# Performance work log

Measured on AMD Instinct MI355X. Metric: run time of the kernel, lower is better.

Reference implementation:

```python
import jax, jax.numpy as jnp
import numpy as np

N = 50000      # nodes
E = 800000     # edges
IN_DIM = 256
HID = 96
OUT = 64
K = 2
ALPHA = 0.15
SCALING = 1.8  # NormalizedGCNConv scaling_factor
EPS = 1e-12    # torch F.normalize eps


def setup_inputs() -> dict:
    key = jax.random.key(0)
    ks = jax.random.split(key, 8)
    x = jax.random.normal(ks[0], (N, IN_DIM), jnp.float32)
    edge_index = jax.random.randint(ks[1], (2, E), 0, N, dtype=jnp.int64)
    def lin(k, fi, fo):
        s = 1.0 / np.sqrt(fi)
        kw, kb = jax.random.split(k)
        W = jax.random.uniform(kw, (fi, fo), jnp.float32, -s, s)
        b = jax.random.uniform(kb, (fo,), jnp.float32, -s, s)
        return W, b
    W0, b0 = lin(ks[2], IN_DIM, HID)   # convs[0]
    W1, b1 = lin(ks[3], HID, HID)      # convs[1]
    Wx, bx = lin(ks[4], HID, OUT)      # convx
    return {"x": x, "edge_index": edge_index,
            "W0": W0, "b0": b0, "W1": W1, "b1": b1, "Wx": Wx, "bx": bx}


def _l2norm(x):
    n = jnp.linalg.norm(x, axis=1, keepdims=True)
    return x / jnp.maximum(n, EPS)


def _gcn_norm(edge_index):
    # add self loops, symmetric normalization D^-1/2 (A+I) D^-1/2
    loop = jnp.arange(N, dtype=edge_index.dtype)
    row = jnp.concatenate([edge_index[0], loop])
    col = jnp.concatenate([edge_index[1], loop])
    deg = jax.ops.segment_sum(jnp.ones(row.shape[0], jnp.float32), col, num_segments=N)
    dinv = jnp.where(deg > 0, jax.lax.rsqrt(jnp.maximum(deg, 1.0)), 0.0)
    norm = dinv[row] * dinv[col]   # [E+N]
    return row, col, norm


def _norm_gcn_conv(x, W, b, row, col, norm):
    # linear -> L2 normalize * 1.8 -> APPNP(K, alpha), eval mode (no dropout)
    x = x @ W + b
    x = _l2norm(x) * SCALING
    h = x
    for _ in range(K):
        agg = jax.ops.segment_sum(x[row] * norm[:, None], col, num_segments=N)
        x = (1.0 - ALPHA) * agg + ALPHA * h
    return x


def reference(x, edge_index, W0, b0, W1, b1, Wx, bx):
    row, col, norm = _gcn_norm(edge_index)
    out = jax.nn.relu(_norm_gcn_conv(x, W0, b0, row, col, norm))
    # depth=3, link_len=2: loop runs i=1 only, residual condition never fires
    out = _l2norm(_norm_gcn_conv(out, W1, b1, row, col, norm)) * 1.5
    return _norm_gcn_conv(out, Wx, bx, row, col, norm)
```

## Files before the change

### kernel.cpp

```cpp
#include <hip/hip_runtime.h>
#include <hip/hip_fp16.h>
#include <math.h>

#define BETA_C 0.85f
#define ALF_C  0.15f
#define SLOTS 48

typedef _Float16 f16x8 __attribute__((ext_vector_type(8)));
typedef float f32x4 __attribute__((ext_vector_type(4)));

__device__ inline f16x8 as_h8(uint4 v) { union { uint4 u; f16x8 h; } U; U.u = v; return U.h; }

__global__ __launch_bounds__(256) void k_fill_tlp(
        const int* __restrict__ row, const int* __restrict__ col,
        int* __restrict__ cur, int* __restrict__ adj, int E, unsigned mulc) {
    int cls = blockIdx.x & 7;
    int e = (blockIdx.x >> 3) * 256 + threadIdx.x;
    if (e >= E) return;
    int c = col[e];
    if ((int)(((unsigned long long)(unsigned)c * mulc) >> 32) != cls) return;
    int p = atomicAdd(&cur[c], 1);
    if (p < SLOTS) adj[(size_t)c * SLOTS + p] = row[e];
}

__global__ void k_prep(const int* __restrict__ cur, float2* __restrict__ dinv2,
                       int* __restrict__ adj, int n, int t0,
                       const float* __restrict__ W0, const float* __restrict__ W1,
                       const float* __restrict__ Wx, ushort* __restrict__ WT0,
                       ushort* __restrict__ WT1, ushort* __restrict__ WTx) {
    int idx = blockIdx.x * blockDim.x + threadIdx.x;
    if (idx < n) {
        int deg = cur[idx];
        float degf = (float)deg + 1.0f;
        dinv2[idx] = make_float2(rsqrtf(degf), ALF_C * sqrtf(degf));
        int ds = min(deg, SLOTS);
        int d4 = (ds + 3) & ~3;
        int* ap = adj + (size_t)idx * SLOTS;
        for (int p = ds; p < d4; ++p) ap[p] = idx;
    } else if (idx >= t0) {
        const int S0 = 96 * 256, S1 = 96 * 96, S2 = 64 * 96;
        int li = idx - t0;
        const float* W; ushort* WT; int FI, FO;
        if (li < S0)           { W = W0; WT = WT0; FI = 256; FO = 96; }
        else if (li < S0 + S1) { W = W1; WT = WT1; FI = 96;  FO = 96; li -= S0; }
        else if (li < S0+S1+S2){ W = Wx; WT = WTx; FI = 96;  FO = 64; li -= S0 + S1; }
        else return;
        int nrow = li / FI, k = li % FI;
        _Float16 hv = (_Float16)W[(size_t)k * FO + nrow];
        WT[li] = *(ushort*)&hv;
    }
}

template<int FI, int FO, int ASRC_F16>
__global__ __launch_bounds__(256) void k_gemm_mfma(
        const void* __restrict__ Xv, const ushort* __restrict__ WT,
        const float* __restrict__ Bias, const float2* __restrict__ dinv2,
        ushort* __restrict__ H, int n, float scale) {
    constexpr int NT = FO / 16;
    constexpr int CPR = FI / 8;
    __shared__ ushort sA[64 * FI];
    __shared__ ushort sW[FO * FI];
    const int tid = threadIdx.x;
    const int rb = blockIdx.x * 64;

    {
        constexpr int TOT = FO * CPR;
#pragma unroll
        for (int idx = tid; idx < TOT; idx += 256) {
            int nrow = idx / CPR, c = idx % CPR;
            uint4 v = *(((const uint4*)WT) + (size_t)nrow * CPR + c);
            int byte = ((nrow * FI + c * 8) * 2) ^ ((nrow & 7) << 4);
            *(uint4*)((char*)sW + byte) = v;
        }
    }
    {
        constexpr int TOT = 64 * CPR;
#pragma unroll
        for (int idx = tid; idx < TOT; idx += 256) {
            int r = idx / CPR, c = idx % CPR;
            int gr = rb + r;
            uint4 v = make_uint4(0u, 0u, 0u, 0u);
            if (ASRC_F16) {
                if (gr < n) v = *(((const uint4*)Xv) + (size_t)gr * CPR + c);
            } else {
                if (gr < n) {
                    const float4* Xp = (const float4*)Xv;
                    float4 f0 = Xp[(size_t)gr * (FI / 4) + c * 2];
                    float4 f1 = Xp[(size_t)gr * (FI / 4) + c * 2 + 1];
                    _Float16 hv[8] = {(_Float16)f0.x, (_Float16)f0.y, (_Float16)f0.z,
                                      (_Float16)f0.w, (_Float16)f1.x, (_Float16)f1.y,
                                      (_Float16)f1.z, (_Float16)f1.w};
                    v = *(uint4*)hv;
                }
            }
            int byte = ((r * FI + c * 8) * 2) ^ ((r & 7) << 4);
            *(uint4*)((char*)sA + byte) = v;
        }
    }
    __syncthreads();

    const int lane = tid & 63;
    const int wave = tid >> 6;
    const int lcol = lane & 15;
    const int lk = lane >> 4;

    f32x4 acc[NT];
#pragma unroll
    for (int t = 0; t < NT; ++t) acc[t] = (f32x4){0.f, 0.f, 0.f, 0.f};

    const int arow = wave * 16 + lcol;
    char* sAb = (char*)sA;
    char* sWb = (char*)sW;
#pragma unroll
    for (int s = 0; s < FI / 32; ++s) {
        int abyte = ((arow * FI + s * 32 + lk * 8) * 2) ^ ((arow & 7) << 4);
        f16x8 af = *(f16x8*)(sAb + abyte);
#pragma unroll
        for (int t = 0; t < NT; ++t) {
            int nrow = t * 16 + lcol;
            int bbyte = ((nrow * FI + s * 32 + lk * 8) * 2) ^ ((nrow & 7) << 4);
            f16x8 bf = *(f16x8*)(sWb + bbyte);
            acc[t] = __builtin_amdgcn_mfma_f32_16x16x32_f16(af, bf, acc[t], 0, 0, 0);
        }
    }

    float bv[NT];
#pragma unroll
    for (int t = 0; t < NT; ++t) bv[t] = Bias[t * 16 + lcol];
    float ss[4] = {0.f, 0.f, 0.f, 0.f};
#pragma unroll
    for (int t = 0; t < NT; ++t)
#pragma unroll
        for (int r = 0; r < 4; ++r) {
            acc[t][r] += bv[t];
            ss[r] += acc[t][r] * acc[t][r];
        }
    for (int m = 1; m < 16; m <<= 1) {
#pragma unroll
        for (int r = 0; r < 4; ++r) ss[r] += __shfl_xor(ss[r], m, 64);
    }
#pragma unroll
    for (int r = 0; r < 4; ++r) {
        int grow = rb + wave * 16 + lk * 4 + r;
        if (grow < n) {
            float sc = scale * dinv2[grow].x / fmaxf(sqrtf(ss[r]), 1e-12f);
#pragma unroll
            for (int t = 0; t < NT; ++t) {
                _Float16 hv = (_Float16)(acc[t][r] * sc);
                H[(size_t)grow * FO + t * 16 + lcol] = *(ushort*)&hv;
            }
        }
    }
}

__device__ inline void unpack8(uint4 v, float* f) {
    union { uint4 u; _Float16 h[8]; } U; U.u = v;
#pragma unroll
    for (int i = 0; i < 8; ++i) f[i] = (float)U.h[i];
}

template<int C8>
__device__ inline void gather_h(const uint4* __restrict__ tab,
                                const int* __restrict__ ap,
                                int d4, int j, f16x8& A0, f16x8& A1) {
    const int4* ap4 = (const int4*)ap;
    int e = 0;
    for (; e + 8 <= d4; e += 8) {
        int4 a0 = ap4[e >> 2];
        int4 a1 = ap4[(e >> 2) + 1];
        uint4 v0 = tab[(size_t)(unsigned)a0.x * C8 + j];
        uint4 v1 = tab[(size_t)(unsigned)a0.y * C8 + j];
        uint4 v2 = tab[(size_t)(unsigned)a0.z * C8 + j];
        uint4 v3 = tab[(size_t)(unsigned)a0.w * C8 + j];
        uint4 v4 = tab[(size_t)(unsigned)a1.x * C8 + j];
        uint4 v5 = tab[(size_t)(unsigned)a1.y * C8 + j];
        uint4 v6 = tab[(size_t)(unsigned)a1.z * C8 + j];
        uint4 v7 = tab[(size_t)(unsigned)a1.w * C8 + j];
        A0 += (as_h8(v0) + as_h8(v1)) + (as_h8(v2) + as_h8(v3));
        A1 += (as_h8(v4) + as_h8(v5)) + (as_h8(v6) + as_h8(v7));
    }
    if (e < d4) {
        int4 a0 = ap4[e >> 2];
        uint4 v0 = tab[(size_t)(unsigned)a0.x * C8 + j];
        uint4 v1 = tab[(size_t)(unsigned)a0.y * C8 + j];
        uint4 v2 = tab[(size_t)(unsigned)a0.z * C8 + j];
        uint4 v3 = tab[(size_t)(unsigned)a0.w * C8 + j];
        A0 += as_h8(v0) + as_h8(v1);
        A1 += as_h8(v2) + as_h8(v3);
    }
}

template<int C8, int TPB>
__global__ __launch_bounds__(TPB) void k_prop1(
        const uint4* __restrict__ y0, uint4* __restrict__ y1,
        const int* __restrict__ adj, const int* __restrict__ cnt,
        const float2* __restrict__ dinv2, int n) {
    int tid = threadIdx.x;
    int j = tid % C8, cl = tid / C8;
    int c = blockIdx.x * (TPB / C8) + cl;
    if (c >= n) return;
    uint4 sv = y0[(size_t)c * C8 + j];
    float d = dinv2[c].x;
    float a = BETA_C * d * d;
    int deg = min(cnt[c], SLOTS);
    int d4 = (deg + 3) & ~3;
    float coef_s = (a + ALF_C) - a * (float)(d4 - deg);
    f16x8 A0 = {0, 0, 0, 0, 0, 0, 0, 0};
    f16x8 A1 = {0, 0, 0, 0, 0, 0, 0, 0};
    gather_h<C8>(y0, adj + (size_t)c * SLOTS, d4, j, A0, A1);
    float sf[8];
    unpack8(sv, sf);
    _Float16 hv[8];
#pragma unroll
    for (int i = 0; i < 8; ++i) {
        float acc = (float)A0[i] + (float)A1[i];
        hv[i] = (_Float16)(a * acc + coef_s * sf[i]);
    }
    y1[(size_t)c * C8 + j] = *(uint4*)hv;
}

template<int C8, int TPB, int ACT, int OUTF32, int NORM>
__global__ __launch_bounds__(TPB) void k_prop2(
        const uint4* __restrict__ y1, const uint4* __restrict__ y0,
        void* __restrict__ out, const int* __restrict__ adj,
        const int* __restrict__ cnt, const float2* __restrict__ dinv2,
        int n, float nscale) {
    __shared__ float ssh[NORM ? TPB : 1];
    int tid = threadIdx.x;
    int j = tid % C8, cl = tid / C8;
    int c = blockIdx.x * (TPB / C8) + cl;
    if (!NORM && c >= n) return;
    bool on = !NORM || c < n;
    float res[8] = {0, 0, 0, 0, 0, 0, 0, 0};
    if (on) {
        uint4 sv1 = y1[(size_t)c * C8 + j];
        uint4 sv0 = y0[(size_t)c * C8 + j];
        float2 dv = dinv2[c];
        float a = BETA_C * dv.x;
        float t = dv.y;
        int deg = min(cnt[c], SLOTS);
        int d4 = (deg + 3) & ~3;
        float coef_s = a * (1.0f - (float)(d4 - deg));
        f16x8 A0 = {0, 0, 0, 0, 0, 0, 0, 0};
        f16x8 A1 = {0, 0, 0, 0, 0, 0, 0, 0};
        gather_h<C8>(y1, adj + (size_t)c * SLOTS, d4, j, A0, A1);
        float sf[8], tf[8];
        unpack8(sv1, sf);
        unpack8(sv0, tf);
#pragma unroll
        for (int i = 0; i < 8; ++i) {
            float acc = (float)A0[i] + (float)A1[i];
            res[i] = a * acc + coef_s * sf[i] + t * tf[i];
            if (ACT) res[i] = fmaxf(res[i], 0.f);
        }
    }
    if (NORM) {
        float part = 0.f;
#pragma unroll
        for (int i = 0; i < 8; ++i) part += res[i] * res[i];
        ssh[tid] = part;
        __syncthreads();
        if (!on) return;
        float tot = 0.f;
#pragma unroll
        for (int q = 0; q < C8; ++q) tot += ssh[cl * C8 + q];
        float sc = nscale / fmaxf(sqrtf(tot), 1e-12f);
        _Float16 hv[8];
#pragma unroll
        for (int i = 0; i < 8; ++i) hv[i] = (_Float16)(res[i] * sc);
        ((uint4*)out)[(size_t)c * C8 + j] = *(uint4*)hv;
    } else if (OUTF32) {
        float4* op = (float4*)out;
        op[(size_t)c * (C8 * 2) + j * 2]     = make_float4(res[0], res[1], res[2], res[3]);
        op[(size_t)c * (C8 * 2) + j * 2 + 1] = make_float4(res[4], res[5], res[6], res[7]);
    } else {
        _Float16 hv[8];
#pragma unroll
        for (int i = 0; i < 8; ++i) hv[i] = (_Float16)res[i];
        ((uint4*)out)[(size_t)c * C8 + j] = *(uint4*)hv;
    }
}

extern "C" void kernel_launch(void* const* d_in, const int* in_sizes, int n_in,
                              void* d_out, int out_size, void* d_ws, size_t ws_size,
                              hipStream_t stream) {
    const float* x  = (const float*)d_in[0];
    const int*   ei = (const int*)d_in[1];
    const float* W0 = (const float*)d_in[2];
    const float* b0 = (const float*)d_in[3];
    const float* W1 = (const float*)d_in[4];
    const float* b1 = (const float*)d_in[5];
    const float* Wx = (const float*)d_in[6];
    const float* bx = (const float*)d_in[7];
    float* out = (float*)d_out;

    const int N = in_sizes[0] / 256;
    const int E = in_sizes[1] / 2;
    const int* row = ei;
    const int* col = ei + E;

    char* ws = (char*)d_ws;
    size_t off = 0;
    auto alloc = [&](size_t bytes) -> char* {
        char* p = ws + off;
        off += (bytes + 255) & ~(size_t)255;
        return p;
    };
    int*    cur   = (int*)alloc((size_t)N * 4);
    float2* dinv2 = (float2*)alloc((size_t)N * 8);
    int*    adj   = (int*)alloc((size_t)N * SLOTS * 4);
    ushort* WT0   = (ushort*)alloc((size_t)96 * 256 * 2);
    ushort* WT1   = (ushort*)alloc((size_t)96 * 96 * 2);
    ushort* WTx   = (ushort*)alloc((size_t)64 * 96 * 2);
    ushort* Hh    = (ushort*)alloc((size_t)N * 96 * 2);
    ushort* T1h   = (ushort*)alloc((size_t)N * 96 * 2);
    ushort* T2h   = (ushort*)alloc((size_t)N * 96 * 2);
    (void)ws_size; (void)n_in; (void)out_size;

    unsigned mulc = (unsigned)((((unsigned long long)8 << 32) + (unsigned)N - 1) / (unsigned)N);

    hipMemsetAsync(cur, 0, (size_t)N * 4, stream);
    {
        int chunks = (E + 255) / 256;
        k_fill_tlp<<<chunks * 8, 256, 0, stream>>>(row, col, cur, adj, E, mulc);
    }
    {
        int t0 = ((N + 255) / 256) * 256;
        int tot = t0 + 96 * 256 + 96 * 96 + 64 * 96;
        k_prep<<<(tot + 255) / 256, 256, 0, stream>>>(cur, dinv2, adj, N, t0,
                                                      W0, W1, Wx, WT0, WT1, WTx);
    }

    int gblk = (N + 63) / 64;
    int gp12 = (N + 15) / 16;
    int gp8  = (N + 31) / 32;

    k_gemm_mfma<256, 96, 0><<<gblk, 256, 0, stream>>>(x, WT0, b0, dinv2, Hh, N, 1.8f);
    k_prop1<12, 192><<<gp12, 192, 0, stream>>>(
        (const uint4*)Hh, (uint4*)T1h, adj, cur, dinv2, N);
    k_prop2<12, 192, 1, 0, 0><<<gp12, 192, 0, stream>>>(
        (const uint4*)T1h, (const uint4*)Hh, T2h, adj, cur, dinv2, N, 0.f);

    k_gemm_mfma<96, 96, 1><<<gblk, 256, 0, stream>>>(T2h, WT1, b1, dinv2, Hh, N, 1.8f);
    k_prop1<12, 192><<<gp12, 192, 0, stream>>>(
        (const uint4*)Hh, (uint4*)T1h, adj, cur, dinv2, N);
    k_prop2<12, 192, 0, 0, 1><<<gp12, 192, 0, stream>>>(
        (const uint4*)T1h, (const uint4*)Hh, T2h, adj, cur, dinv2, N, 1.5f);

    k_gemm_mfma<96, 64, 1><<<gblk, 256, 0, stream>>>(T2h, WTx, bx, dinv2, Hh, N, 1.8f);
    k_prop1<8, 256><<<gp8, 256, 0, stream>>>(
        (const uint4*)Hh, (uint4*)T1h, adj, cur, dinv2, N);
    k_prop2<8, 256, 0, 1, 0><<<gp8, 256, 0, stream>>>(
        (const uint4*)T1h, (const uint4*)Hh, out, adj, cur, dinv2, N, 0.f);
}
```

Measured before the change: 219.1 us.

## Fuse second propagation step with following layer GEMM via shared-memory staging

```diff
diff --git a/kernel.cpp b/kernel.cpp
--- a/kernel.cpp
+++ b/kernel.cpp
@@ -8,8 +8,15 @@
 
 typedef _Float16 f16x8 __attribute__((ext_vector_type(8)));
 typedef float f32x4 __attribute__((ext_vector_type(4)));
+typedef int i32x4 __attribute__((ext_vector_type(4)));
 
 __device__ inline f16x8 as_h8(uint4 v) { union { uint4 u; f16x8 h; } U; U.u = v; return U.h; }
+
+__device__ inline void unpack8(uint4 v, float* f) {
+    union { uint4 u; _Float16 h[8]; } U; U.u = v;
+#pragma unroll
+    for (int i = 0; i < 8; ++i) f[i] = (float)U.h[i];
+}
 
 __global__ __launch_bounds__(256) void k_fill_tlp(
         const int* __restrict__ row, const int* __restrict__ col,
@@ -51,9 +58,9 @@
     }
 }
 
-template<int FI, int FO, int ASRC_F16>
+template<int FI, int FO>
 __global__ __launch_bounds__(256) void k_gemm_mfma(
-        const void* __restrict__ Xv, const ushort* __restrict__ WT,
+        const float* __restrict__ X, const ushort* __restrict__ WT,
         const float* __restrict__ Bias, const float2* __restrict__ dinv2,
         ushort* __restrict__ H, int n, float scale) {
     constexpr int NT = FO / 16;
@@ -80,18 +87,14 @@
             int r = idx / CPR, c = idx % CPR;
             int gr = rb + r;
             uint4 v = make_uint4(0u, 0u, 0u, 0u);
-            if (ASRC_F16) {
-                if (gr < n) v = *(((const uint4*)Xv) + (size_t)gr * CPR + c);
-            } else {
-                if (gr < n) {
-                    const float4* Xp = (const float4*)Xv;
-                    float4 f0 = Xp[(size_t)gr * (FI / 4) + c * 2];
-                    float4 f1 = Xp[(size_t)gr * (FI / 4) + c * 2 + 1];
-                    _Float16 hv[8] = {(_Float16)f0.x, (_Float16)f0.y, (_Float16)f0.z,
-                                      (_Float16)f0.w, (_Float16)f1.x, (_Float16)f1.y,
-                                      (_Float16)f1.z, (_Float16)f1.w};
-                    v = *(uint4*)hv;
-                }
+            if (gr < n) {
+                const float4* Xp = (const float4*)X;
+                float4 f0 = Xp[(size_t)gr * (FI / 4) + c * 2];
+                float4 f1 = Xp[(size_t)gr * (FI / 4) + c * 2 + 1];
+                _Float16 hv[8] = {(_Float16)f0.x, (_Float16)f0.y, (_Float16)f0.z,
+                                  (_Float16)f0.w, (_Float16)f1.x, (_Float16)f1.y,
+                                  (_Float16)f1.z, (_Float16)f1.w};
+                v = *(uint4*)hv;
             }
             int byte = ((r * FI + c * 8) * 2) ^ ((r & 7) << 4);
             *(uint4*)((char*)sA + byte) = v;
@@ -153,38 +156,31 @@
     }
 }
 
-__device__ inline void unpack8(uint4 v, float* f) {
-    union { uint4 u; _Float16 h[8]; } U; U.u = v;
-#pragma unroll
-    for (int i = 0; i < 8; ++i) f[i] = (float)U.h[i];
-}
-
 template<int C8>
 __device__ inline void gather_h(const uint4* __restrict__ tab,
                                 const int* __restrict__ ap,
                                 int d4, int j, f16x8& A0, f16x8& A1) {
-    const int4* ap4 = (const int4*)ap;
     int e = 0;
     for (; e + 8 <= d4; e += 8) {
-        int4 a0 = ap4[e >> 2];
-        int4 a1 = ap4[(e >> 2) + 1];
-        uint4 v0 = tab[(size_t)(unsigned)a0.x * C8 + j];
-        uint4 v1 = tab[(size_t)(unsigned)a0.y * C8 + j];
-        uint4 v2 = tab[(size_t)(unsigned)a0.z * C8 + j];
-        uint4 v3 = tab[(size_t)(unsigned)a0.w * C8 + j];
-        uint4 v4 = tab[(size_t)(unsigned)a1.x * C8 + j];
-        uint4 v5 = tab[(size_t)(unsigned)a1.y * C8 + j];
-        uint4 v6 = tab[(size_t)(unsigned)a1.z * C8 + j];
-        uint4 v7 = tab[(size_t)(unsigned)a1.w * C8 + j];
+        i32x4 a0 = __builtin_nontemporal_load((const i32x4*)ap + (e >> 2));
+        i32x4 a1 = __builtin_nontemporal_load((const i32x4*)ap + (e >> 2) + 1);
+        uint4 v0 = tab[(size_t)(unsigned)a0[0] * C8 + j];
+        uint4 v1 = tab[(size_t)(unsigned)a0[1] * C8 + j];
+        uint4 v2 = tab[(size_t)(unsigned)a0[2] * C8 + j];
+        uint4 v3 = tab[(size_t)(unsigned)a0[3] * C8 + j];
+        uint4 v4 = tab[(size_t)(unsigned)a1[0] * C8 + j];
+        uint4 v5 = tab[(size_t)(unsigned)a1[1] * C8 + j];
+        uint4 v6 = tab[(size_t)(unsigned)a1[2] * C8 + j];
+        uint4 v7 = tab[(size_t)(unsigned)a1[3] * C8 + j];
         A0 += (as_h8(v0) + as_h8(v1)) + (as_h8(v2) + as_h8(v3));
         A1 += (as_h8(v4) + as_h8(v5)) + (as_h8(v6) + as_h8(v7));
     }
     if (e < d4) {
-        int4 a0 = ap4[e >> 2];
-        uint4 v0 = tab[(size_t)(unsigned)a0.x * C8 + j];
-        uint4 v1 = tab[(size_t)(unsigned)a0.y * C8 + j];
-        uint4 v2 = tab[(size_t)(unsigned)a0.z * C8 + j];
-        uint4 v3 = tab[(size_t)(unsigned)a0.w * C8 + j];
+        i32x4 a0 = __builtin_nontemporal_load((const i32x4*)ap + (e >> 2));
+        uint4 v0 = tab[(size_t)(unsigned)a0[0] * C8 + j];
+        uint4 v1 = tab[(size_t)(unsigned)a0[1] * C8 + j];
+        uint4 v2 = tab[(size_t)(unsigned)a0[2] * C8 + j];
+        uint4 v3 = tab[(size_t)(unsigned)a0[3] * C8 + j];
         A0 += as_h8(v0) + as_h8(v1);
         A1 += as_h8(v2) + as_h8(v3);
     }
@@ -219,65 +215,200 @@
     y1[(size_t)c * C8 + j] = *(uint4*)hv;
 }
 
-template<int C8, int TPB, int ACT, int OUTF32, int NORM>
-__global__ __launch_bounds__(TPB) void k_prop2(
+template<int C8, int TPB>
+__global__ __launch_bounds__(TPB) void k_prop2_out(
         const uint4* __restrict__ y1, const uint4* __restrict__ y0,
-        void* __restrict__ out, const int* __restrict__ adj,
-        const int* __restrict__ cnt, const float2* __restrict__ dinv2,
-        int n, float nscale) {
-    __shared__ float ssh[NORM ? TPB : 1];
+        float4* __restrict__ out, const int* __restrict__ adj,
+        const int* __restrict__ cnt, const float2* __restrict__ dinv2, int n) {
     int tid = threadIdx.x;
     int j = tid % C8, cl = tid / C8;
     int c = blockIdx.x * (TPB / C8) + cl;
-    if (!NORM && c >= n) return;
-    bool on = !NORM || c < n;
-    float res[8] = {0, 0, 0, 0, 0, 0, 0, 0};
-    if (on) {
-        uint4 sv1 = y1[(size_t)c * C8 + j];
-        uint4 sv0 = y0[(size_t)c * C8 + j];
-        float2 dv = dinv2[c];
-        float a = BETA_C * dv.x;
-        float t = dv.y;
-        int deg = min(cnt[c], SLOTS);
-        int d4 = (deg + 3) & ~3;
-        float coef_s = a * (1.0f - (float)(d4 - deg));
-        f16x8 A0 = {0, 0, 0, 0, 0, 0, 0, 0};
-        f16x8 A1 = {0, 0, 0, 0, 0, 0, 0, 0};
-        gather_h<C8>(y1, adj + (size_t)c * SLOTS, d4, j, A0, A1);
-        float sf[8], tf[8];
-        unpack8(sv1, sf);
-        unpack8(sv0, tf);
-#pragma unroll
-        for (int i = 0; i < 8; ++i) {
-            float acc = (float)A0[i] + (float)A1[i];
-            res[i] = a * acc + coef_s * sf[i] + t * tf[i];
-            if (ACT) res[i] = fmaxf(res[i], 0.f);
-        }
-    }
-    if (NORM) {
-        float part = 0.f;
-#pragma unroll
-        for (int i = 0; i < 8; ++i) part += res[i] * res[i];
-        ssh[tid] = part;
-        __syncthreads();
-        if (!on) return;
-        float tot = 0.f;
-#pragma unroll
-        for (int q = 0; q < C8; ++q) tot += ssh[cl * C8 + q];
-        float sc = nscale / fmaxf(sqrtf(tot), 1e-12f);
-        _Float16 hv[8];
-#pragma unroll
-        for (int i = 0; i < 8; ++i) hv[i] = (_Float16)(res[i] * sc);
-        ((uint4*)out)[(size_t)c * C8 + j] = *(uint4*)hv;
-    } else if (OUTF32) {
-        float4* op = (float4*)out;
-        op[(size_t)c * (C8 * 2) + j * 2]     = make_float4(res[0], res[1], res[2], res[3]);
-        op[(size_t)c * (C8 * 2) + j * 2 + 1] = make_float4(res[4], res[5], res[6], res[7]);
-    } else {
-        _Float16 hv[8];
-#pragma unroll
-        for (int i = 0; i < 8; ++i) hv[i] = (_Float16)res[i];
-        ((uint4*)out)[(size_t)c * C8 + j] = *(uint4*)hv;
+    if (c >= n) return;
+    uint4 sv1 = y1[(size_t)c * C8 + j];
+    uint4 sv0 = y0[(size_t)c * C8 + j];
+    float2 dv = dinv2[c];
+    float a = BETA_C * dv.x;
+    float t = dv.y;
+    int deg = min(cnt[c], SLOTS);
+    int d4 = (deg + 3) & ~3;
+    float coef_s = a * (1.0f - (float)(d4 - deg));
+    f16x8 A0 = {0, 0, 0, 0, 0, 0, 0, 0};
+    f16x8 A1 = {0, 0, 0, 0, 0, 0, 0, 0};
+    gather_h<C8>(y1, adj + (size_t)c * SLOTS, d4, j, A0, A1);
+    float sf[8], tf[8];
+    unpack8(sv1, sf);
+    unpack8(sv0, tf);
+    float res[8];
+#pragma unroll
+    for (int i = 0; i < 8; ++i) {
+        float acc = (float)A0[i] + (float)A1[i];
+        res[i] = a * acc + coef_s * sf[i] + t * tf[i];
+    }
+    out[(size_t)c * (C8 * 2) + j * 2]     = make_float4(res[0], res[1], res[2], res[3]);
+    out[(size_t)c * (C8 * 2) + j * 2 + 1] = make_float4(res[4], res[5], res[6], res[7]);
+}
+
+template<int FO, int ACT, int NORM>
+__global__ __launch_bounds__(256) void k_prop2_gemm(
+        const uint4* __restrict__ y1, const uint4* __restrict__ y0,
+        const int* __restrict__ adj, const int* __restrict__ cnt,
+        const float2* __restrict__ dinv2,
+        const ushort* __restrict__ WT, const float* __restrict__ Bias,
+        ushort* __restrict__ H, int n, float nscale, float gscale) {
+    constexpr int FI = 96;
+    constexpr int CPR = 12;
+    constexpr int NT = FO / 16;
+    __shared__ ushort sA[64 * FI];
+    __shared__ ushort sW[FO * FI];
+    __shared__ float ssh[NORM ? 256 : 1];
+    const int tid = threadIdx.x;
+    const int rb = blockIdx.x * 64;
+
+#pragma unroll
+    for (int idx = tid; idx < FO * CPR; idx += 256) {
+        int nrow = idx / CPR, cc = idx % CPR;
+        uint4 v = *(((const uint4*)WT) + (size_t)nrow * CPR + cc);
+        int byte = ((nrow * FI + cc * 8) * 2) ^ ((nrow & 7) << 4);
+        *(uint4*)((char*)sW + byte) = v;
+    }
+
+    {
+        int cl = tid >> 2, jl = tid & 3;
+        int c = rb + cl;
+        bool on = c < n;
+        float res[3][8];
+#pragma unroll
+        for (int k = 0; k < 3; ++k)
+#pragma unroll
+            for (int i = 0; i < 8; ++i) res[k][i] = 0.f;
+        if (on) {
+            float2 dv = dinv2[c];
+            float a = BETA_C * dv.x;
+            float t = dv.y;
+            int deg = min(cnt[c], SLOTS);
+            int d4 = (deg + 3) & ~3;
+            float coef_s = a * (1.0f - (float)(d4 - deg));
+            const int* ap = adj + (size_t)c * SLOTS;
+            uint4 sv1[3], sv0[3];
+#pragma unroll
+            for (int k = 0; k < 3; ++k) {
+                sv1[k] = y1[(size_t)c * CPR + jl + k * 4];
+                sv0[k] = y0[(size_t)c * CPR + jl + k * 4];
+            }
+            f16x8 A0[3], A1[3];
+#pragma unroll
+            for (int k = 0; k < 3; ++k) {
+                A0[k] = (f16x8){0, 0, 0, 0, 0, 0, 0, 0};
+                A1[k] = (f16x8){0, 0, 0, 0, 0, 0, 0, 0};
+            }
+            for (int e = 0; e + 4 <= d4; e += 4) {
+                i32x4 av = __builtin_nontemporal_load((const i32x4*)ap + (e >> 2));
+                uint4 v0[3], v1[3], v2[3], v3[3];
+#pragma unroll
+                for (int k = 0; k < 3; ++k) {
+                    v0[k] = y1[(size_t)(unsigned)av[0] * CPR + jl + k * 4];
+                    v1[k] = y1[(size_t)(unsigned)av[1] * CPR + jl + k * 4];
+                    v2[k] = y1[(size_t)(unsigned)av[2] * CPR + jl + k * 4];
+                    v3[k] = y1[(size_t)(unsigned)av[3] * CPR + jl + k * 4];
+                }
+#pragma unroll
+                for (int k = 0; k < 3; ++k) {
+                    A0[k] += as_h8(v0[k]) + as_h8(v1[k]);
+                    A1[k] += as_h8(v2[k]) + as_h8(v3[k]);
+                }
+            }
+#pragma unroll
+            for (int k = 0; k < 3; ++k) {
+                float sf[8], tf[8];
+                unpack8(sv1[k], sf);
+                unpack8(sv0[k], tf);
+#pragma unroll
+                for (int i = 0; i < 8; ++i) {
+                    float acc = (float)A0[k][i] + (float)A1[k][i];
+                    float r = a * acc + coef_s * sf[i] + t * tf[i];
+                    if (ACT) r = fmaxf(r, 0.f);
+                    res[k][i] = r;
+                }
+            }
+        }
+        if (NORM) {
+            float part = 0.f;
+#pragma unroll
+            for (int k = 0; k < 3; ++k)
+#pragma unroll
+                for (int i = 0; i < 8; ++i) part += res[k][i] * res[k][i];
+            ssh[tid] = part;
+            __syncthreads();
+            float tot = ssh[cl * 4] + ssh[cl * 4 + 1] + ssh[cl * 4 + 2] + ssh[cl * 4 + 3];
+            float sc = nscale / fmaxf(sqrtf(tot), 1e-12f);
+#pragma unroll
+            for (int k = 0; k < 3; ++k)
+#pragma unroll
+                for (int i = 0; i < 8; ++i) res[k][i] *= sc;
+        }
+#pragma unroll
+        for (int k = 0; k < 3; ++k) {
+            _Float16 hv[8];
+#pragma unroll
+            for (int i = 0; i < 8; ++i) hv[i] = (_Float16)res[k][i];
+            int ch = jl + k * 4;
+            int byte = ((cl * FI + ch * 8) * 2) ^ ((cl & 7) << 4);
+            *(uint4*)((char*)sA + byte) = *(uint4*)hv;
+        }
+    }
+    __syncthreads();
+
+    const int lane = tid & 63;
+    const int wave = tid >> 6;
+    const int lcol = lane & 15;
+    const int lk = lane >> 4;
+
+    f32x4 acc[NT];
+#pragma unroll
+    for (int t = 0; t < NT; ++t) acc[t] = (f32x4){0.f, 0.f, 0.f, 0.f};
+
+    const int arow = wave * 16 + lcol;
+    char* sAb = (char*)sA;
+    char* sWb = (char*)sW;
+#pragma unroll
+    for (int s = 0; s < FI / 32; ++s) {
+        int abyte = ((arow * FI + s * 32 + lk * 8) * 2) ^ ((arow & 7) << 4);
+        f16x8 af = *(f16x8*)(sAb + abyte);
+#pragma unroll
+        for (int t = 0; t < NT; ++t) {
+            int nrow = t * 16 + lcol;
+            int bbyte = ((nrow * FI + s * 32 + lk * 8) * 2) ^ ((nrow & 7) << 4);
+            f16x8 bf = *(f16x8*)(sWb + bbyte);
+            acc[t] = __builtin_amdgcn_mfma_f32_16x16x32_f16(af, bf, acc[t], 0, 0, 0);
+        }
+    }
+
+    float bv[NT];
+#pragma unroll
+    for (int t = 0; t < NT; ++t) bv[t] = Bias[t * 16 + lcol];
+    float ss[4] = {0.f, 0.f, 0.f, 0.f};
+#pragma unroll
+    for (int t = 0; t < NT; ++t)
+#pragma unroll
+        for (int r = 0; r < 4; ++r) {
+            acc[t][r] += bv[t];
+            ss[r] += acc[t][r] * acc[t][r];
+        }
+    for (int m = 1; m < 16; m <<= 1) {
+#pragma unroll
+        for (int r = 0; r < 4; ++r) ss[r] += __shfl_xor(ss[r], m, 64);
+    }
+#pragma unroll
+    for (int r = 0; r < 4; ++r) {
+        int grow = rb + wave * 16 + lk * 4 + r;
+        if (grow < n) {
+            float sc = gscale * dinv2[grow].x / fmaxf(sqrtf(ss[r]), 1e-12f);
+#pragma unroll
+            for (int t = 0; t < NT; ++t) {
+                _Float16 hv = (_Float16)(acc[t][r] * sc);
+                H[(size_t)grow * FO + t * 16 + lcol] = *(ushort*)&hv;
+            }
+        }
     }
 }
 
@@ -314,7 +445,7 @@
     ushort* WTx   = (ushort*)alloc((size_t)64 * 96 * 2);
     ushort* Hh    = (ushort*)alloc((size_t)N * 96 * 2);
     ushort* T1h   = (ushort*)alloc((size_t)N * 96 * 2);
-    ushort* T2h   = (ushort*)alloc((size_t)N * 96 * 2);
+    ushort* Gh    = (ushort*)alloc((size_t)N * 96 * 2);
     (void)ws_size; (void)n_in; (void)out_size;
 
     unsigned mulc = (unsigned)((((unsigned long long)8 << 32) + (unsigned)N - 1) / (unsigned)N);
@@ -335,21 +466,19 @@
     int gp12 = (N + 15) / 16;
     int gp8  = (N + 31) / 32;
 
-    k_gemm_mfma<256, 96, 0><<<gblk, 256, 0, stream>>>(x, WT0, b0, dinv2, Hh, N, 1.8f);
+    k_gemm_mfma<256, 96><<<gblk, 256, 0, stream>>>(x, WT0, b0, dinv2, Hh, N, 1.8f);
     k_prop1<12, 192><<<gp12, 192, 0, stream>>>(
         (const uint4*)Hh, (uint4*)T1h, adj, cur, dinv2, N);
-    k_prop2<12, 192, 1, 0, 0><<<gp12, 192, 0, stream>>>(
-        (const uint4*)T1h, (const uint4*)Hh, T2h, adj, cur, dinv2, N, 0.f);
-
-    k_gemm_mfma<96, 96, 1><<<gblk, 256, 0, stream>>>(T2h, WT1, b1, dinv2, Hh, N, 1.8f);
+    k_prop2_gemm<96, 1, 0><<<gblk, 256, 0, stream>>>(
+        (const uint4*)T1h, (const uint4*)Hh, adj, cur, dinv2, WT1, b1, Gh, N, 0.f, 1.8f);
+
     k_prop1<12, 192><<<gp12, 192, 0, stream>>>(
-        (const uint4*)Hh, (uint4*)T1h, adj, cur, dinv2, N);
-    k_prop2<12, 192, 0, 0, 1><<<gp12, 192, 0, stream>>>(
-        (const uint4*)T1h, (const uint4*)Hh, T2h, adj, cur, dinv2, N, 1.5f);
-
-    k_gemm_mfma<96, 64, 1><<<gblk, 256, 0, stream>>>(T2h, WTx, bx, dinv2, Hh, N, 1.8f);
+        (const uint4*)Gh, (uint4*)T1h, adj, cur, dinv2, N);
+    k_prop2_gemm<64, 0, 1><<<gblk, 256, 0, stream>>>(
+        (const uint4*)T1h, (const uint4*)Gh, adj, cur, dinv2, WTx, bx, Hh, N, 1.5f, 1.8f);
+
     k_prop1<8, 256><<<gp8, 256, 0, stream>>>(
         (const uint4*)Hh, (uint4*)T1h, adj, cur, dinv2, N);
-    k_prop2<8, 256, 0, 1, 0><<<gp8, 256, 0, stream>>>(
-        (const uint4*)T1h, (const uint4*)Hh, out, adj, cur, dinv2, N, 0.f);
-}
+    k_prop2_out<8, 256><<<gp8, 256, 0, stream>>>(
+        (const uint4*)T1h, (const uint4*)Hh, (float4*)out, adj, cur, dinv2, N);
+}
```

Result: slower. 233.1 us (+6.4%).

## Split feature tables into 32-column planes and gather per plane with nontemporal hints

Applied to the files above, without the earlier changes.

```diff
diff --git a/kernel.cpp b/kernel.cpp
--- a/kernel.cpp
+++ b/kernel.cpp
@@ -8,8 +8,22 @@
 
 typedef _Float16 f16x8 __attribute__((ext_vector_type(8)));
 typedef float f32x4 __attribute__((ext_vector_type(4)));
+typedef int i32x4 __attribute__((ext_vector_type(4)));
+typedef unsigned int u32x4 __attribute__((ext_vector_type(4)));
 
 __device__ inline f16x8 as_h8(uint4 v) { union { uint4 u; f16x8 h; } U; U.u = v; return U.h; }
+__device__ inline f16x8 as_h8v(u32x4 v) { union { u32x4 u; f16x8 h; } U; U.u = v; return U.h; }
+
+__device__ inline void unpack8(uint4 v, float* f) {
+    union { uint4 u; _Float16 h[8]; } U; U.u = v;
+#pragma unroll
+    for (int i = 0; i < 8; ++i) f[i] = (float)U.h[i];
+}
+__device__ inline void unpack8v(u32x4 v, float* f) {
+    union { u32x4 u; _Float16 h[8]; } U; U.u = v;
+#pragma unroll
+    for (int i = 0; i < 8; ++i) f[i] = (float)U.h[i];
+}
 
 __global__ __launch_bounds__(256) void k_fill_tlp(
         const int* __restrict__ row, const int* __restrict__ col,
@@ -62,6 +76,7 @@
     __shared__ ushort sW[FO * FI];
     const int tid = threadIdx.x;
     const int rb = blockIdx.x * 64;
+    const size_t SUB4 = (size_t)n * 4;
 
     {
         constexpr int TOT = FO * CPR;
@@ -81,7 +96,10 @@
             int gr = rb + r;
             uint4 v = make_uint4(0u, 0u, 0u, 0u);
             if (ASRC_F16) {
-                if (gr < n) v = *(((const uint4*)Xv) + (size_t)gr * CPR + c);
+                if (gr < n) {
+                    int pass = c >> 2, off = c & 3;
+                    v = ((const uint4*)Xv)[(size_t)pass * SUB4 + (size_t)gr * 4 + off];
+                }
             } else {
                 if (gr < n) {
                     const float4* Xp = (const float4*)Xv;
@@ -139,6 +157,7 @@
 #pragma unroll
         for (int r = 0; r < 4; ++r) ss[r] += __shfl_xor(ss[r], m, 64);
     }
+    const size_t SUBH = (size_t)n * 32;
 #pragma unroll
     for (int r = 0; r < 4; ++r) {
         int grow = rb + wave * 16 + lk * 4 + r;
@@ -146,138 +165,150 @@
             float sc = scale * dinv2[grow].x / fmaxf(sqrtf(ss[r]), 1e-12f);
 #pragma unroll
             for (int t = 0; t < NT; ++t) {
+                int colc = t * 16 + lcol;
                 _Float16 hv = (_Float16)(acc[t][r] * sc);
-                H[(size_t)grow * FO + t * 16 + lcol] = *(ushort*)&hv;
+                H[(size_t)(colc >> 5) * SUBH + (size_t)grow * 32 + (colc & 31)] = *(ushort*)&hv;
             }
         }
     }
 }
 
-__device__ inline void unpack8(uint4 v, float* f) {
-    union { uint4 u; _Float16 h[8]; } U; U.u = v;
-#pragma unroll
-    for (int i = 0; i < 8; ++i) f[i] = (float)U.h[i];
-}
-
-template<int C8>
-__device__ inline void gather_h(const uint4* __restrict__ tab,
+__device__ inline void gather64(const uint4* __restrict__ tp,
                                 const int* __restrict__ ap,
-                                int d4, int j, f16x8& A0, f16x8& A1) {
-    const int4* ap4 = (const int4*)ap;
+                                int d4, int jl, f16x8& A0, f16x8& A1) {
     int e = 0;
     for (; e + 8 <= d4; e += 8) {
-        int4 a0 = ap4[e >> 2];
-        int4 a1 = ap4[(e >> 2) + 1];
-        uint4 v0 = tab[(size_t)(unsigned)a0.x * C8 + j];
-        uint4 v1 = tab[(size_t)(unsigned)a0.y * C8 + j];
-        uint4 v2 = tab[(size_t)(unsigned)a0.z * C8 + j];
-        uint4 v3 = tab[(size_t)(unsigned)a0.w * C8 + j];
-        uint4 v4 = tab[(size_t)(unsigned)a1.x * C8 + j];
-        uint4 v5 = tab[(size_t)(unsigned)a1.y * C8 + j];
-        uint4 v6 = tab[(size_t)(unsigned)a1.z * C8 + j];
-        uint4 v7 = tab[(size_t)(unsigned)a1.w * C8 + j];
+        i32x4 a0 = __builtin_nontemporal_load((const i32x4*)ap + (e >> 2));
+        i32x4 a1 = __builtin_nontemporal_load((const i32x4*)ap + (e >> 2) + 1);
+        uint4 v0 = tp[(size_t)(unsigned)a0[0] * 4 + jl];
+        uint4 v1 = tp[(size_t)(unsigned)a0[1] * 4 + jl];
+        uint4 v2 = tp[(size_t)(unsigned)a0[2] * 4 + jl];
+        uint4 v3 = tp[(size_t)(unsigned)a0[3] * 4 + jl];
+        uint4 v4 = tp[(size_t)(unsigned)a1[0] * 4 + jl];
+        uint4 v5 = tp[(size_t)(unsigned)a1[1] * 4 + jl];
+        uint4 v6 = tp[(size_t)(unsigned)a1[2] * 4 + jl];
+        uint4 v7 = tp[(size_t)(unsigned)a1[3] * 4 + jl];
         A0 += (as_h8(v0) + as_h8(v1)) + (as_h8(v2) + as_h8(v3));
         A1 += (as_h8(v4) + as_h8(v5)) + (as_h8(v6) + as_h8(v7));
     }
     if (e < d4) {
-        int4 a0 = ap4[e >> 2];
-        uint4 v0 = tab[(size_t)(unsigned)a0.x * C8 + j];
-        uint4 v1 = tab[(size_t)(unsigned)a0.y * C8 + j];
-        uint4 v2 = tab[(size_t)(unsigned)a0.z * C8 + j];
-        uint4 v3 = tab[(size_t)(unsigned)a0.w * C8 + j];
+        i32x4 a0 = __builtin_nontemporal_load((const i32x4*)ap + (e >> 2));
+        uint4 v0 = tp[(size_t)(unsigned)a0[0] * 4 + jl];
+        uint4 v1 = tp[(size_t)(unsigned)a0[1] * 4 + jl];
+        uint4 v2 = tp[(size_t)(unsigned)a0[2] * 4 + jl];
+        uint4 v3 = tp[(size_t)(unsigned)a0[3] * 4 + jl];
         A0 += as_h8(v0) + as_h8(v1);
         A1 += as_h8(v2) + as_h8(v3);
     }
 }
 
-template<int C8, int TPB>
-__global__ __launch_bounds__(TPB) void k_prop1(
+template<int P>
+__global__ __launch_bounds__(256) void k_prop1b(
         const uint4* __restrict__ y0, uint4* __restrict__ y1,
         const int* __restrict__ adj, const int* __restrict__ cnt,
         const float2* __restrict__ dinv2, int n) {
     int tid = threadIdx.x;
-    int j = tid % C8, cl = tid / C8;
-    int c = blockIdx.x * (TPB / C8) + cl;
+    int jl = tid & 3, cl = tid >> 2;
+    int c = blockIdx.x * 64 + cl;
     if (c >= n) return;
-    uint4 sv = y0[(size_t)c * C8 + j];
+    const size_t SUB4 = (size_t)n * 4;
     float d = dinv2[c].x;
     float a = BETA_C * d * d;
     int deg = min(cnt[c], SLOTS);
     int d4 = (deg + 3) & ~3;
     float coef_s = (a + ALF_C) - a * (float)(d4 - deg);
-    f16x8 A0 = {0, 0, 0, 0, 0, 0, 0, 0};
-    f16x8 A1 = {0, 0, 0, 0, 0, 0, 0, 0};
-    gather_h<C8>(y0, adj + (size_t)c * SLOTS, d4, j, A0, A1);
-    float sf[8];
-    unpack8(sv, sf);
-    _Float16 hv[8];
-#pragma unroll
-    for (int i = 0; i < 8; ++i) {
-        float acc = (float)A0[i] + (float)A1[i];
-        hv[i] = (_Float16)(a * acc + coef_s * sf[i]);
-    }
-    y1[(size_t)c * C8 + j] = *(uint4*)hv;
-}
-
-template<int C8, int TPB, int ACT, int OUTF32, int NORM>
-__global__ __launch_bounds__(TPB) void k_prop2(
+    const int* ap = adj + (size_t)c * SLOTS;
+    const size_t selfi = (size_t)c * 4 + jl;
+#pragma unroll
+    for (int p = 0; p < P; ++p) {
+        const uint4* tp = y0 + (size_t)p * SUB4;
+        uint4 sv = tp[selfi];
+        f16x8 A0 = {0, 0, 0, 0, 0, 0, 0, 0};
+        f16x8 A1 = {0, 0, 0, 0, 0, 0, 0, 0};
+        gather64(tp, ap, d4, jl, A0, A1);
+        float sf[8];
+        unpack8(sv, sf);
+        _Float16 hv[8];
+#pragma unroll
+        for (int i = 0; i < 8; ++i) {
+            float acc = (float)A0[i] + (float)A1[i];
+            hv[i] = (_Float16)(a * acc + coef_s * sf[i]);
+        }
+        __builtin_nontemporal_store(*(u32x4*)hv, (u32x4*)y1 + (size_t)p * SUB4 + selfi);
+    }
+}
+
+template<int P, int ACT, int NORM, int OUTF32>
+__global__ __launch_bounds__(256) void k_prop2b(
         const uint4* __restrict__ y1, const uint4* __restrict__ y0,
-        void* __restrict__ out, const int* __restrict__ adj,
+        void* __restrict__ outv, const int* __restrict__ adj,
         const int* __restrict__ cnt, const float2* __restrict__ dinv2,
         int n, float nscale) {
-    __shared__ float ssh[NORM ? TPB : 1];
     int tid = threadIdx.x;
-    int j = tid % C8, cl = tid / C8;
-    int c = blockIdx.x * (TPB / C8) + cl;
-    if (!NORM && c >= n) return;
-    bool on = !NORM || c < n;
-    float res[8] = {0, 0, 0, 0, 0, 0, 0, 0};
-    if (on) {
-        uint4 sv1 = y1[(size_t)c * C8 + j];
-        uint4 sv0 = y0[(size_t)c * C8 + j];
-        float2 dv = dinv2[c];
-        float a = BETA_C * dv.x;
-        float t = dv.y;
-        int deg = min(cnt[c], SLOTS);
-        int d4 = (deg + 3) & ~3;
-        float coef_s = a * (1.0f - (float)(d4 - deg));
+    int jl = tid & 3, cl = tid >> 2;
+    int c = blockIdx.x * 64 + cl;
+    if (c >= n) return;
+    const size_t SUB4 = (size_t)n * 4;
+    float2 dv = dinv2[c];
+    float a = BETA_C * dv.x;
+    float t = dv.y;
+    int deg = min(cnt[c], SLOTS);
+    int d4 = (deg + 3) & ~3;
+    float coef_s = a * (1.0f - (float)(d4 - deg));
+    const int* ap = adj + (size_t)c * SLOTS;
+    const size_t selfi = (size_t)c * 4 + jl;
+
+    float res[P][8];
+#pragma unroll
+    for (int p = 0; p < P; ++p) {
+        const uint4* tp = y1 + (size_t)p * SUB4;
+        uint4 sv1 = tp[selfi];
+        u32x4 sv0 = __builtin_nontemporal_load((const u32x4*)y0 + (size_t)p * SUB4 + selfi);
         f16x8 A0 = {0, 0, 0, 0, 0, 0, 0, 0};
         f16x8 A1 = {0, 0, 0, 0, 0, 0, 0, 0};
-        gather_h<C8>(y1, adj + (size_t)c * SLOTS, d4, j, A0, A1);
+        gather64(tp, ap, d4, jl, A0, A1);
         float sf[8], tf[8];
         unpack8(sv1, sf);
-        unpack8(sv0, tf);
+        unpack8v(sv0, tf);
 #pragma unroll
         for (int i = 0; i < 8; ++i) {
             float acc = (float)A0[i] + (float)A1[i];
-            res[i] = a * acc + coef_s * sf[i] + t * tf[i];
-            if (ACT) res[i] = fmaxf(res[i], 0.f);
+            float r = a * acc + coef_s * sf[i] + t * tf[i];
+            if (ACT) r = fmaxf(r, 0.f);
+            res[p][i] = r;
+        }
+        if (!NORM) {
+            if (OUTF32) {
+                float4* op = (float4*)outv;
+                size_t base = (size_t)c * (P * 8) + p * 8 + jl * 2;
+                op[base]     = make_float4(res[p][0], res[p][1], res[p][2], res[p][3]);
+                op[base + 1] = make_float4(res[p][4], res[p][5], res[p][6], res[p][7]);
+            } else {
+                _Float16 hv[8];
+#pragma unroll
+                for (int i = 0; i < 8; ++i) hv[i] = (_Float16)res[p][i];
+                __builtin_nontemporal_store(*(u32x4*)hv,
+                                            (u32x4*)outv + (size_t)p * SUB4 + selfi);
+            }
         }
     }
     if (NORM) {
-        float part = 0.f;
-#pragma unroll
-        for (int i = 0; i < 8; ++i) part += res[i] * res[i];
-        ssh[tid] = part;
-        __syncthreads();
-        if (!on) return;
-        float tot = 0.f;
-#pragma unroll
-        for (int q = 0; q < C8; ++q) tot += ssh[cl * C8 + q];
-        float sc = nscale / fmaxf(sqrtf(tot), 1e-12f);
-        _Float16 hv[8];
-#pragma unroll
-        for (int i = 0; i < 8; ++i) hv[i] = (_Float16)(res[i] * sc);
-        ((uint4*)out)[(size_t)c * C8 + j] = *(uint4*)hv;
-    } else if (OUTF32) {
-        float4* op = (float4*)out;
-        op[(size_t)c * (C8 * 2) + j * 2]     = make_float4(res[0], res[1], res[2], res[3]);
-        op[(size_t)c * (C8 * 2) + j * 2 + 1] = make_float4(res[4], res[5], res[6], res[7]);
-    } else {
-        _Float16 hv[8];
-#pragma unroll
-        for (int i = 0; i < 8; ++i) hv[i] = (_Float16)res[i];
-        ((uint4*)out)[(size_t)c * C8 + j] = *(uint4*)hv;
+        float ss = 0.f;
+#pragma unroll
+        for (int p = 0; p < P; ++p)
+#pragma unroll
+            for (int i = 0; i < 8; ++i) ss += res[p][i] * res[p][i];
+        ss += __shfl_xor(ss, 1, 64);
+        ss += __shfl_xor(ss, 2, 64);
+        float sc = nscale / fmaxf(sqrtf(ss), 1e-12f);
+#pragma unroll
+        for (int p = 0; p < P; ++p) {
+            _Float16 hv[8];
+#pragma unroll
+            for (int i = 0; i < 8; ++i) hv[i] = (_Float16)(res[p][i] * sc);
+            __builtin_nontemporal_store(*(u32x4*)hv,
+                                        (u32x4*)outv + (size_t)p * SUB4 + selfi);
+        }
     }
 }
 
@@ -312,9 +343,10 @@
     ushort* WT0   = (ushort*)alloc((size_t)96 * 256 * 2);
     ushort* WT1   = (ushort*)alloc((size_t)96 * 96 * 2);
     ushort* WTx   = (ushort*)alloc((size_t)64 * 96 * 2);
-    ushort* Hh    = (ushort*)alloc((size_t)N * 96 * 2);
-    ushort* T1h   = (ushort*)alloc((size_t)N * 96 * 2);
-    ushort* T2h   = (ushort*)alloc((size_t)N * 96 * 2);
+    ushort* Hb    = (ushort*)alloc((size_t)N * 96 * 2);
+    ushort* T1b   = (ushort*)alloc((size_t)N * 96 * 2);
+    ushort* T2b   = (ushort*)alloc((size_t)N * 96 * 2);
+    ushort* Gb    = (ushort*)alloc((size_t)N * 96 * 2);
     (void)ws_size; (void)n_in; (void)out_size;
 
     unsigned mulc = (unsigned)((((unsigned long long)8 << 32) + (unsigned)N - 1) / (unsigned)N);
@@ -332,24 +364,22 @@
     }
 
     int gblk = (N + 63) / 64;
-    int gp12 = (N + 15) / 16;
-    int gp8  = (N + 31) / 32;
-
-    k_gemm_mfma<256, 96, 0><<<gblk, 256, 0, stream>>>(x, WT0, b0, dinv2, Hh, N, 1.8f);
-    k_prop1<12, 192><<<gp12, 192, 0, stream>>>(
-        (const uint4*)Hh, (uint4*)T1h, adj, cur, dinv2, N);
-    k_prop2<12, 192, 1, 0, 0><<<gp12, 192, 0, stream>>>(
-        (const uint4*)T1h, (const uint4*)Hh, T2h, adj, cur, dinv2, N, 0.f);
-
-    k_gemm_mfma<96, 96, 1><<<gblk, 256, 0, stream>>>(T2h, WT1, b1, dinv2, Hh, N, 1.8f);
-    k_prop1<12, 192><<<gp12, 192, 0, stream>>>(
-        (const uint4*)Hh, (uint4*)T1h, adj, cur, dinv2, N);
-    k_prop2<12, 192, 0, 0, 1><<<gp12, 192, 0, stream>>>(
-        (const uint4*)T1h, (const uint4*)Hh, T2h, adj, cur, dinv2, N, 1.5f);
-
-    k_gemm_mfma<96, 64, 1><<<gblk, 256, 0, stream>>>(T2h, WTx, bx, dinv2, Hh, N, 1.8f);
-    k_prop1<8, 256><<<gp8, 256, 0, stream>>>(
-        (const uint4*)Hh, (uint4*)T1h, adj, cur, dinv2, N);
-    k_prop2<8, 256, 0, 1, 0><<<gp8, 256, 0, stream>>>(
-        (const uint4*)T1h, (const uint4*)Hh, out, adj, cur, dinv2, N, 0.f);
-}
+
+    k_gemm_mfma<256, 96, 0><<<gblk, 256, 0, stream>>>(x, WT0, b0, dinv2, Hb, N, 1.8f);
+    k_prop1b<3><<<gblk, 256, 0, stream>>>(
+        (const uint4*)Hb, (uint4*)T1b, adj, cur, dinv2, N);
+    k_prop2b<3, 1, 0, 0><<<gblk, 256, 0, stream>>>(
+        (const uint4*)T1b, (const uint4*)Hb, T2b, adj, cur, dinv2, N, 0.f);
+
+    k_gemm_mfma<96, 96, 1><<<gblk, 256, 0, stream>>>(T2b, WT1, b1, dinv2, Gb, N, 1.8f);
+    k_prop1b<3><<<gblk, 256, 0, stream>>>(
+        (const uint4*)Gb, (uint4*)T1b, adj, cur, dinv2, N);
+    k_prop2b<3, 0, 1, 0><<<gblk, 256, 0, stream>>>(
+        (const uint4*)T1b, (const uint4*)Gb, T2b, adj, cur, dinv2, N, 1.5f);
+
+    k_gemm_mfma<96, 64, 1><<<gblk, 256, 0, stream>>>(T2b, WTx, bx, dinv2, Hb, N, 1.8f);
+    k_prop1b<2><<<gblk, 256, 0, stream>>>(
+        (const uint4*)Hb, (uint4*)T1b, adj, cur, dinv2, N);
+    k_prop2b<2, 0, 0, 1><<<gblk, 256, 0, stream>>>(
+        (const uint4*)T1b, (const uint4*)Hb, out, adj, cur, dinv2, N, 0.f);
+}
```

Result: slower. 288.0 us (+31.4%).
